# Kernel optimization log

Measured on AMD Instinct MI355X. Metric: run time of the kernel, lower is better.

The kernel has to match this reference:

```python
import jax, jax.numpy as jnp
import numpy as np
import math

L, D, H, DK, DFF, B, S = 4, 512, 8, 256, 2048, 8, 256
HD = H * DK
EPS = 1e-6


def _norm(x, alpha, bias):
    # torch: alpha*(x-mean)/(std_unbiased + eps) + bias  (std uses ddof=1)
    mu = x.mean(axis=-1, keepdims=True)
    var = ((x - mu) ** 2).sum(axis=-1, keepdims=True) / (x.shape[-1] - 1)
    return alpha * (x - mu) / (jnp.sqrt(var) + EPS) + bias


def _positional_encoding():
    pos = jnp.arange(S, dtype=jnp.float32)[:, None]          # [S,1]
    i = jnp.arange(0, D, 2, dtype=jnp.float32)               # even indices
    pe_sin = jnp.sin(pos / (S ** (2.0 * i / D)))             # [S,D/2]
    pe_cos = jnp.cos(pos / (S ** (2.0 * (i + 1.0) / D)))     # [S,D/2]
    pe = jnp.zeros((S, D), dtype=jnp.float32)
    pe = pe.at[:, 0::2].set(pe_sin).at[:, 1::2].set(pe_cos)
    return pe


def setup_inputs() -> dict:
    key = jax.random.key(0)
    ks = jax.random.split(key, 16)
    sc = 0.02
    inp = {
        "data": jax.random.normal(ks[0], (B, S, D), dtype=jnp.float32),
        "attn_m": jax.random.randint(ks[1], (B, S), 0, 2, dtype=jnp.int32),
        "view_idx": 0,
        "seg_emb": jax.random.normal(ks[2], (3, D), dtype=jnp.float32) * sc,
        "Wq": jax.random.normal(ks[3], (L, D, HD), dtype=jnp.float32) * sc,
        "bq": jnp.zeros((L, HD), dtype=jnp.float32),
        "Wk": jax.random.normal(ks[4], (L, D, HD), dtype=jnp.float32) * sc,
        "bk": jnp.zeros((L, HD), dtype=jnp.float32),
        "Wv": jax.random.normal(ks[5], (L, D, HD), dtype=jnp.float32) * sc,
        "bv": jnp.zeros((L, HD), dtype=jnp.float32),
        "Wo": jax.random.normal(ks[6], (L, HD, D), dtype=jnp.float32) * sc,
        "bo": jnp.zeros((L, D), dtype=jnp.float32),
        "W1": jax.random.normal(ks[7], (L, D, DFF), dtype=jnp.float32) * sc,
        "b1": jnp.zeros((L, DFF), dtype=jnp.float32),
        "W2": jax.random.normal(ks[8], (L, DFF, D), dtype=jnp.float32) * sc,
        "b2": jnp.zeros((L, D), dtype=jnp.float32),
        "alpha1": jnp.ones((L, D), dtype=jnp.float32),
        "bias1": jnp.zeros((L, D), dtype=jnp.float32),
        "alpha2": jnp.ones((L, D), dtype=jnp.float32),
        "bias2": jnp.zeros((L, D), dtype=jnp.float32),
        "alpha_f": jnp.ones((D,), dtype=jnp.float32),
        "bias_f": jnp.zeros((D,), dtype=jnp.float32),
    }
    return inp


def reference(data, attn_m, view_idx, seg_emb, Wq, bq, Wk, bk, Wv, bv, Wo, bo,
              W1, b1, W2, b2, alpha1, bias1, alpha2, bias2, alpha_f, bias_f):
    # positional encoder: x*sqrt(d_f) + pe + seg_embedding(view_idx*seq_len)
    pe = _positional_encoding()
    seg_idx = view_idx * S  # scalar; must be < 3 (view_idx == 0 in practice)
    x = data * math.sqrt(D) + pe[None, :, :] + seg_emb[seg_idx][None, None, :]

    # mask: attn_m [B,S] -> [B,1,1,S] bool, True = masked (key axis)
    maskb = attn_m.astype(bool)[:, None, None, :]

    for i in range(L):
        x2 = _norm(x, alpha1[i], bias1[i])
        q = (x2 @ Wq[i] + bq[i]).reshape(B, S, H, DK).transpose(0, 2, 1, 3)
        k = (x2 @ Wk[i] + bk[i]).reshape(B, S, H, DK).transpose(0, 2, 1, 3)
        v = (x2 @ Wv[i] + bv[i]).reshape(B, S, H, DK).transpose(0, 2, 1, 3)
        scores = jnp.einsum('bhqd,bhkd->bhqk', q, k) / math.sqrt(DK)
        scores = jnp.where(maskb, -1e9, scores)
        attnw = jax.nn.softmax(scores, axis=-1)
        o = jnp.einsum('bhqk,bhkd->bhqd', attnw, v)
        o = o.transpose(0, 2, 1, 3).reshape(B, S, HD) @ Wo[i] + bo[i]
        x = x + o
        x2 = _norm(x, alpha2[i], bias2[i])
        ff = jax.nn.relu(x2 @ W1[i] + b1[i]) @ W2[i] + b2[i]
        x = x + ff

    return _norm(x, alpha_f, bias_f)
```

## Files before the change

kernel.cpp:

```cpp
#include <hip/hip_runtime.h>
#include <hip/hip_bf16.h>

#define LNUM 4
#define DIM  512
#define SS   256

typedef unsigned short ushort_t;
typedef __attribute__((ext_vector_type(8))) short bf16x8;
typedef __attribute__((ext_vector_type(4))) float f32x4;
typedef __attribute__((ext_vector_type(8))) unsigned short u16x8;

#define VWAIT(n) asm volatile("s_waitcnt vmcnt(" #n ")" ::: "memory")
#define LWAIT()  asm volatile("s_waitcnt lgkmcnt(0)" ::: "memory")
__device__ __forceinline__ void bar() { __builtin_amdgcn_s_barrier(); }

__device__ __forceinline__ ushort_t f2b(float f) {
  union { float f; unsigned u; } x; x.f = f;
  unsigned r = x.u + 0x7FFFu + ((x.u >> 16) & 1u);
  return (ushort_t)(r >> 16);
}

__device__ __forceinline__ void gload16(const void* g, void* s) {
  __builtin_amdgcn_global_load_lds((const __attribute__((address_space(1))) void*)g,
                                   (__attribute__((address_space(3))) void*)s, 16, 0, 0);
}

template<int TM, int TN, int EPI, int NBUF>
__global__ __launch_bounds__(256, 2)
void gemm_bt(const ushort_t* __restrict__ A, const ushort_t* __restrict__ B,
             const float* __restrict__ bias, const float* __restrict__ bias2,
             const float* __restrict__ bias3,
             ushort_t* __restrict__ outB, ushort_t* __restrict__ outB2,
             ushort_t* __restrict__ outB3, float* __restrict__ outF,
             int K, int lda, int ldb, int ldc, int nkz, int relu)
{
  constexpr int CA = TM / 32, CB = TN / 32, SN = CA + CB;
  constexpr int WM = TM / 32, WN = TN / 32;
  __shared__ ushort_t As[NBUF * TM * 64];
  __shared__ ushort_t Bs[NBUF * TN * 64];
  const int tid = threadIdx.x, lane = tid & 63, wid = tid >> 6;
  const int wm = wid >> 1, wn = wid & 1;
  const int kz = blockIdx.z;
  const int Kz = K / nkz, k0 = kz * Kz, nt = Kz >> 6;

  const ushort_t* Ab = A + (long)blockIdx.y * TM * lda + k0;
  const ushort_t* Bb = B + (long)blockIdx.x * TN * ldb + k0;

  const ushort_t* srcA[CA]; ushort_t* ldsA[CA];
  const ushort_t* srcB[CB]; ushort_t* ldsB[CB];
#pragma unroll
  for (int c = 0; c < CA; ++c) {
    int off = c * 4096 + tid * 16;
    int row = off >> 7;
    int scol = ((off & 127) ^ ((row & 7) << 4)) >> 1;
    srcA[c] = Ab + (long)row * lda + scol;
    ldsA[c] = As + c * 2048 + wid * 512;
  }
#pragma unroll
  for (int c = 0; c < CB; ++c) {
    int off = c * 4096 + tid * 16;
    int row = off >> 7;
    int scol = ((off & 127) ^ ((row & 7) << 4)) >> 1;
    srcB[c] = Bb + (long)row * ldb + scol;
    ldsB[c] = Bs + c * 2048 + wid * 512;
  }

  f32x4 acc[WM][WN] = {};

  auto STAGE = [&](int buf, int t) {
#pragma unroll
    for (int c = 0; c < CA; ++c) gload16(srcA[c] + t * 64, ldsA[c] + buf * TM * 64);
#pragma unroll
    for (int c = 0; c < CB; ++c) gload16(srcB[c] + t * 64, ldsB[c] + buf * TN * 64);
  };

  auto COMPUTE = [&](int buf) {
#pragma unroll
    for (int ks = 0; ks < 2; ++ks) {
      const int kb = ks * 64 + ((lane >> 4) << 4);
      bf16x8 af[WM], bfr[WN];
#pragma unroll
      for (int f = 0; f < WM; ++f) {
        int ra = wm * (TM / 2) + f * 16 + (lane & 15);
        af[f] = *(const bf16x8*)((const char*)As + buf * TM * 128 + ra * 128 + (kb ^ ((ra & 7) << 4)));
      }
#pragma unroll
      for (int g = 0; g < WN; ++g) {
        int rb = wn * (TN / 2) + g * 16 + (lane & 15);
        bfr[g] = *(const bf16x8*)((const char*)Bs + buf * TN * 128 + rb * 128 + (kb ^ ((rb & 7) << 4)));
      }
      __builtin_amdgcn_s_setprio(1);
#pragma unroll
      for (int i = 0; i < WM; ++i)
#pragma unroll
        for (int j = 0; j < WN; ++j)
          acc[i][j] = __builtin_amdgcn_mfma_f32_16x16x32_bf16(af[i], bfr[j], acc[i][j], 0, 0, 0);
      __builtin_amdgcn_s_setprio(0);
    }
  };

  STAGE(0, 0);
  if constexpr (NBUF == 3) {
    STAGE(1, 1);
    for (int t = 0; t < nt; ++t) {
      if (t < nt - 1) { if constexpr (SN == 6) VWAIT(6); else VWAIT(4); }
      else VWAIT(0);
      bar();
      if (t + 2 < nt) STAGE((t + 2) % 3, t + 2);
      COMPUTE(t % 3);
    }
  } else {
    for (int t = 0; t < nt; ++t) {
      VWAIT(0);
      bar();
      if (t + 1 < nt) STAGE((t + 1) & 1, t + 1);
      COMPUTE(t & 1);
    }
  }

  const int row0 = blockIdx.y * TM + wm * (TM / 2) + ((lane >> 4) << 2);
  int col0 = blockIdx.x * TN + wn * (TN / 2) + (lane & 15);
  const float* bsel = bias;
  ushort_t* osel = outB;
  int seg = 0;
  if (EPI == 3) {
    seg = (blockIdx.x * TN) >> 11;
    if (seg == 1) { bsel = bias2; osel = outB2; }
    else if (seg == 2) { bsel = bias3; }
    col0 -= seg * 2048;
  }

  if (EPI == 3 && seg == 2) {
    ushort_t* Vt = As;
    const int colvBase = blockIdx.x * TN - 4096;
    const int rowBase = blockIdx.y * TM;
    const int h = colvBase >> 8, dk0 = colvBase & 255;
    const int bh = ((rowBase >> 8) << 3) + h;
    const int s0 = rowBase & 255;
    bar();
#pragma unroll
    for (int half = 0; half < 2; ++half) {
      if (half) bar();
      if (wn == half) {
#pragma unroll
        for (int i = 0; i < WM; ++i)
#pragma unroll
          for (int j = 0; j < WN; ++j) {
            const int colL = j * 16 + (lane & 15);
            const float bv = bsel[col0 + j * 16];
#pragma unroll
            for (int r = 0; r < 4; ++r) {
              const int rowL = wm * 64 + i * 16 + ((lane >> 4) << 2) + r;
              Vt[colL * 136 + rowL] = f2b(acc[i][j][r] + bv);
            }
          }
      }
      bar();
      const int dkl = tid >> 2, scc = (tid & 3) * 32;
      ushort_t* dst = outB3 + ((long)bh << 16) +
                      (long)(dk0 + half * 64 + dkl) * 256 + s0 + scc;
#pragma unroll
      for (int m = 0; m < 4; ++m)
        *(u16x8*)(dst + m * 8) = *(const u16x8*)(Vt + dkl * 136 + scc + m * 8);
    }
    return;
  }

#pragma unroll
  for (int i = 0; i < WM; ++i) {
#pragma unroll
    for (int j = 0; j < WN; ++j) {
      const int col = col0 + j * 16;
      float bv = 0.f;
      if (EPI == 2) bv = (kz == 0) ? bias[col] : 0.f;
      else if (EPI == 0 || EPI == 3) bv = bsel[col];
#pragma unroll
      for (int r = 0; r < 4; ++r) {
        const int row = row0 + i * 16 + r;
        float v = acc[i][j][r] + bv;
        if (EPI == 2) {
          outF[(long)kz * 1048576 + (long)row * ldc + col] = v;
        } else if (EPI == 3) {
          const long addr = (((long)(row >> 8) * 8 + (col >> 8)) << 16) +
                            (long)(row & 255) * 256 + (col & 255);
          osel[addr] = f2b(v);
        } else {
          if (relu) v = fmaxf(v, 0.f);
          osel[(long)row * ldc + col] = f2b(v);
        }
      }
    }
  }
}

__global__ __launch_bounds__(256, 2)
void attnf_k(const ushort_t* __restrict__ qh, const ushort_t* __restrict__ kh,
             const ushort_t* __restrict__ vT, const int* __restrict__ attnm,
             ushort_t* __restrict__ ao)
{
  __shared__ ushort_t As[2][64 * 64];
  __shared__ ushort_t Bs[2][256 * 64];
  const int bh = blockIdx.x, qt = blockIdx.y;
  const int b = bh >> 3, h = bh & 7;
  const int tid = threadIdx.x, lane = tid & 63, wid = tid >> 6;
  const int l15 = lane & 15, l4 = lane >> 4;

  unsigned mbits = 0;
#pragma unroll
  for (int j = 0; j < 16; ++j)
    mbits |= (attnm[b * 256 + j * 16 + l15] != 0 ? 1u : 0u) << j;

  const ushort_t* Qb = qh + ((long)bh << 16) + qt * 64 * 256;
  const ushort_t* Kb = kh + ((long)bh << 16);
  const ushort_t* srcA[2]; ushort_t* ldsA[2];
  const ushort_t* srcB[8]; ushort_t* ldsB[8];
#pragma unroll
  for (int c = 0; c < 2; ++c) {
    int off = c * 4096 + tid * 16;
    int row = off >> 7;
    int scol = ((off & 127) ^ ((row & 7) << 4)) >> 1;
    srcA[c] = Qb + (long)row * 256 + scol;
    ldsA[c] = As[0] + c * 2048 + wid * 512;
  }
#pragma unroll
  for (int c = 0; c < 8; ++c) {
    int off = c * 4096 + tid * 16;
    int row = off >> 7;
    int scol = ((off & 127) ^ ((row & 7) << 4)) >> 1;
    srcB[c] = Kb + (long)row * 256 + scol;
    ldsB[c] = Bs[0] + c * 2048 + wid * 512;
  }

  auto STAGE = [&](int buf, int t) {
#pragma unroll
    for (int c = 0; c < 2; ++c) gload16(srcA[c] + t * 64, ldsA[c] + buf * 4096);
#pragma unroll
    for (int c = 0; c < 8; ++c) gload16(srcB[c] + t * 64, ldsB[c] + buf * 16384);
  };

  const ushort_t* Vb = vT + ((long)bh << 16);
  int velem[8];
#pragma unroll
  for (int c = 0; c < 8; ++c) {
    int off = c * 4096 + tid * 16;
    int row = off >> 9;
    int colb = (off & 511) ^ ((row & 7) << 4);
    velem[c] = row * 256 + (colb >> 1);
  }
  auto VSTAGE = [&](int buf, int ch) {
#pragma unroll
    for (int c = 0; c < 8; ++c)
      gload16(Vb + (long)ch * 16384 + velem[c], Bs[buf] + c * 2048 + wid * 512);
  };

  f32x4 sacc[16] = {};
  STAGE(0, 0);
  for (int t = 0; t < 4; ++t) {
    VWAIT(0);
    bar();
    if (t < 3) STAGE((t + 1) & 1, t + 1);
    else       VSTAGE(0, 0);
    const int buf = t & 1;
#pragma unroll
    for (int ks = 0; ks < 2; ++ks) {
      const int kb = ks * 64 + (l4 << 4);
      const int ra = wid * 16 + l15;
      bf16x8 af = *(const bf16x8*)((const char*)As[buf] + ra * 128 + (kb ^ ((ra & 7) << 4)));
      __builtin_amdgcn_s_setprio(1);
#pragma unroll
      for (int j = 0; j < 16; ++j) {
        const int rb = j * 16 + l15;
        bf16x8 bf_ = *(const bf16x8*)((const char*)Bs[buf] + rb * 128 + (kb ^ ((rb & 7) << 4)));
        sacc[j] = __builtin_amdgcn_mfma_f32_16x16x32_bf16(af, bf_, sacc[j], 0, 0, 0);
      }
      __builtin_amdgcn_s_setprio(0);
    }
  }

  float mr[4] = {-3e38f, -3e38f, -3e38f, -3e38f}, sr[4] = {};
#pragma unroll
  for (int j = 0; j < 16; ++j) {
    const bool mk = (mbits >> j) & 1;
#pragma unroll
    for (int r = 0; r < 4; ++r) {
      float s = mk ? -1e9f : sacc[j][r] * 0.0625f;
      sacc[j][r] = s;
      mr[r] = fmaxf(mr[r], s);
    }
  }
#pragma unroll
  for (int o = 1; o < 16; o <<= 1)
#pragma unroll
    for (int r = 0; r < 4; ++r) mr[r] = fmaxf(mr[r], __shfl_xor(mr[r], o, 16));
#pragma unroll
  for (int j = 0; j < 16; ++j)
#pragma unroll
    for (int r = 0; r < 4; ++r) {
      float e = __expf(sacc[j][r] - mr[r]);
      sacc[j][r] = e;
      sr[r] += e;
    }
#pragma unroll
  for (int o = 1; o < 16; o <<= 1)
#pragma unroll
    for (int r = 0; r < 4; ++r) sr[r] += __shfl_xor(sr[r], o, 16);
#pragma unroll
  for (int r = 0; r < 4; ++r) sr[r] = 1.f / sr[r];

  bar();
  ushort_t* Rp = (ushort_t*)Bs[1];
#pragma unroll
  for (int j = 0; j < 16; ++j)
#pragma unroll
    for (int r = 0; r < 4; ++r) {
      const int row = wid * 16 + l4 * 4 + r;
      *(ushort_t*)((char*)Rp + row * 512 + (((j * 16 + l15) * 2) ^ ((row & 7) << 4))) =
          f2b(sacc[j][r] * sr[r]);
    }
  bf16x8 pf[8];
  {
    const int ra = wid * 16 + l15;
#pragma unroll
    for (int ks = 0; ks < 8; ++ks)
      pf[ks] = *(const bf16x8*)((const char*)Rp + ra * 512 +
                                ((ks * 64 + (l4 << 4)) ^ ((ra & 7) << 4)));
  }
  LWAIT();
  VWAIT(0);
  bar();

  f32x4 oacc[16] = {};
  for (int ch = 0; ch < 4; ++ch) {
    if (ch) { VWAIT(0); bar(); }
    if (ch < 3) VSTAGE((ch + 1) & 1, ch + 1);
    const char* vb = (const char*)Bs[ch & 1];
#pragma unroll
    for (int ks = 0; ks < 8; ++ks) {
      const int kb = ks * 64 + (l4 << 4);
      __builtin_amdgcn_s_setprio(1);
#pragma unroll
      for (int j = 0; j < 4; ++j) {
        const int rb = j * 16 + l15;
        bf16x8 vf = *(const bf16x8*)(vb + rb * 512 + (kb ^ ((rb & 7) << 4)));
        oacc[ch * 4 + j] = __builtin_amdgcn_mfma_f32_16x16x32_bf16(pf[ks], vf, oacc[ch * 4 + j], 0, 0, 0);
      }
      __builtin_amdgcn_s_setprio(0);
    }
  }

  const int rowq = qt * 64 + wid * 16 + (l4 << 2);
#pragma unroll
  for (int ch = 0; ch < 4; ++ch)
#pragma unroll
    for (int j = 0; j < 4; ++j) {
      const int dk = ch * 64 + j * 16 + l15;
#pragma unroll
      for (int r = 0; r < 4; ++r)
        ao[(long)(b * 256 + rowq + r) * 2048 + h * 256 + dk] = f2b(oacc[ch * 4 + j][r]);
    }
}

__global__ __launch_bounds__(256)
void build_ln(const float* __restrict__ data, const float* __restrict__ seg,
              const int* __restrict__ viewp,
              const float* __restrict__ alpha, const float* __restrict__ beta,
              float* __restrict__ x, ushort_t* __restrict__ x2)
{
  const int row = blockIdx.x, tid = threadIdx.x;
  const long base = (long)row * DIM;
  const int s = row & 255;
  const int vrow = viewp[0] * SS;
  const int d0 = tid * 2;
  float2 v;
  {
    float2 dv = ((const float2*)(data + base))[tid];
    float a0 = (float)s * exp2f((float)d0 * -0.03125f);
    float a1 = (float)s * exp2f((float)(d0 + 1) * -0.03125f);
    float pe0 = (d0 & 1) ? cosf(a0) : sinf(a0);
    float pe1 = ((d0 + 1) & 1) ? cosf(a1) : sinf(a1);
    v.x = dv.x * 22.627416997969522f + pe0 + seg[vrow * DIM + d0];
    v.y = dv.y * 22.627416997969522f + pe1 + seg[vrow * DIM + d0 + 1];
    ((float2*)(x + base))[tid] = v;
  }
  float sm = v.x + v.y;
#pragma unroll
  for (int o = 32; o; o >>= 1) sm += __shfl_xor(sm, o, 64);
  __shared__ float rs[4], rq[4];
  if ((tid & 63) == 0) rs[tid >> 6] = sm;
  __syncthreads();
  const float mu = (rs[0] + rs[1] + rs[2] + rs[3]) * (1.f / 512.f);
  const float dx = v.x - mu, dy = v.y - mu;
  float q = dx * dx + dy * dy;
#pragma unroll
  for (int o = 32; o; o >>= 1) q += __shfl_xor(q, o, 64);
  if ((tid & 63) == 0) rq[tid >> 6] = q;
  __syncthreads();
  const float var = (rq[0] + rq[1] + rq[2] + rq[3]) * (1.f / 511.f);
  const float rstd = 1.f / (sqrtf(var) + 1e-6f);
  x2[base + d0]     = f2b(alpha[d0] * dx * rstd + beta[d0]);
  x2[base + d0 + 1] = f2b(alpha[d0 + 1] * dy * rstd + beta[d0 + 1]);
}

__global__ __launch_bounds__(256)
void lnorm_k(const float* __restrict__ x, const float* __restrict__ parts, int np,
             float* __restrict__ xout,
             const float* __restrict__ alpha, const float* __restrict__ beta,
             ushort_t* __restrict__ outB, float* __restrict__ outF)
{
  const int row = blockIdx.x, tid = threadIdx.x;
  const long base = (long)row * DIM;
  float2 v = ((const float2*)(x + base))[tid];
  if (np) {
    for (int p = 0; p < np; ++p) {
      float2 a = ((const float2*)(parts + (long)p * 1048576 + base))[tid];
      v.x += a.x; v.y += a.y;
    }
    ((float2*)(xout + base))[tid] = v;
  }
  float s = v.x + v.y;
#pragma unroll
  for (int o = 32; o; o >>= 1) s += __shfl_xor(s, o, 64);
  __shared__ float rs[4], rq[4];
  if ((tid & 63) == 0) rs[tid >> 6] = s;
  __syncthreads();
  const float mu = (rs[0] + rs[1] + rs[2] + rs[3]) * (1.f / 512.f);
  const float dx = v.x - mu, dy = v.y - mu;
  float q = dx * dx + dy * dy;
#pragma unroll
  for (int o = 32; o; o >>= 1) q += __shfl_xor(q, o, 64);
  if ((tid & 63) == 0) rq[tid >> 6] = q;
  __syncthreads();
  const float var = (rq[0] + rq[1] + rq[2] + rq[3]) * (1.f / 511.f);
  const float rstd = 1.f / (sqrtf(var) + 1e-6f);
  const int d0 = tid * 2;
  const float o0 = alpha[d0] * dx * rstd + beta[d0];
  const float o1 = alpha[d0 + 1] * dy * rstd + beta[d0 + 1];
  if (outB) { outB[base + d0] = f2b(o0); outB[base + d0 + 1] = f2b(o1); }
  else      { outF[base + d0] = o0;      outF[base + d0 + 1] = o1; }
}

__global__ __launch_bounds__(256)
void wtransA(const float* __restrict__ Wq, const float* __restrict__ Wk,
             const float* __restrict__ Wv, const float* __restrict__ W1,
             ushort_t* __restrict__ qkvW, ushort_t* __restrict__ W1T)
{
  __shared__ float t[32][33];
  const int z = blockIdx.z, widx = z >> 2, layer = z & 3;
  const float* src = (widx == 0) ? Wq : (widx == 1) ? Wk : (widx == 2) ? Wv : W1;
  src += (long)layer * 512 * 2048;
  ushort_t* dst = (widx == 3) ? (W1T + (long)layer * 2048 * 512)
                              : (qkvW + (long)layer * (6144L * 512) + (long)widx * 2048 * 512);
  const int c0 = blockIdx.x * 32, r0 = blockIdx.y * 32;
  const int tx = threadIdx.x & 31, ty = threadIdx.x >> 5;
#pragma unroll
  for (int i = 0; i < 4; ++i) t[ty + i * 8][tx] = src[(long)(r0 + ty + i * 8) * 2048 + c0 + tx];
  __syncthreads();
#pragma unroll
  for (int i = 0; i < 4; ++i) dst[(long)(c0 + ty + i * 8) * 512 + r0 + tx] = f2b(t[tx][ty + i * 8]);
}

__global__ __launch_bounds__(256)
void wtransB(const float* __restrict__ Wo, const float* __restrict__ W2,
             ushort_t* __restrict__ WoT, ushort_t* __restrict__ W2T)
{
  __shared__ float t[32][33];
  const int z = blockIdx.z, widx = z >> 2, layer = z & 3;
  const float* src = ((widx == 0) ? Wo : W2) + (long)layer * 2048 * 512;
  ushort_t* dst = ((widx == 0) ? WoT : W2T) + (long)layer * 512 * 2048;
  const int c0 = blockIdx.x * 32, r0 = blockIdx.y * 32;
  const int tx = threadIdx.x & 31, ty = threadIdx.x >> 5;
#pragma unroll
  for (int i = 0; i < 4; ++i) t[ty + i * 8][tx] = src[(long)(r0 + ty + i * 8) * 512 + c0 + tx];
  __syncthreads();
#pragma unroll
  for (int i = 0; i < 4; ++i) dst[(long)(c0 + ty + i * 8) * 2048 + r0 + tx] = f2b(t[tx][ty + i * 8]);
}

extern "C" void kernel_launch(void* const* d_in, const int* in_sizes, int n_in,
                              void* d_out, int out_size, void* d_ws, size_t ws_size,
                              hipStream_t stream)
{
  const float* data  = (const float*)d_in[0];
  const int*   attnm = (const int*)d_in[1];
  const int*   viewp = (const int*)d_in[2];
  const float* seg   = (const float*)d_in[3];
  const float* Wq    = (const float*)d_in[4];
  const float* bq    = (const float*)d_in[5];
  const float* Wk    = (const float*)d_in[6];
  const float* bk    = (const float*)d_in[7];
  const float* Wv    = (const float*)d_in[8];
  const float* bv    = (const float*)d_in[9];
  const float* Wo    = (const float*)d_in[10];
  const float* bo    = (const float*)d_in[11];
  const float* W1    = (const float*)d_in[12];
  const float* b1    = (const float*)d_in[13];
  const float* W2    = (const float*)d_in[14];
  const float* b2    = (const float*)d_in[15];
  const float* al1   = (const float*)d_in[16];
  const float* be1   = (const float*)d_in[17];
  const float* al2   = (const float*)d_in[18];
  const float* be2   = (const float*)d_in[19];
  const float* alf   = (const float*)d_in[20];
  const float* bef   = (const float*)d_in[21];

  char* w = (char*)d_ws;
  const size_t MB = 1024 * 1024;
  ushort_t* qkvW = (ushort_t*)(w + 0 * MB);
  ushort_t* WoT  = (ushort_t*)(w + 24 * MB);
  ushort_t* W1T  = (ushort_t*)(w + 32 * MB);
  ushort_t* W2T  = (ushort_t*)(w + 40 * MB);
  float*    x    = (float*)   (w + 48 * MB);
  ushort_t* x2   = (ushort_t*)(w + 52 * MB);
  ushort_t* qb   = (ushort_t*)(w + 54 * MB);
  ushort_t* kbf  = (ushort_t*)(w + 62 * MB);
  ushort_t* vT   = (ushort_t*)(w + 70 * MB);
  ushort_t* ao   = (ushort_t*)(w + 78 * MB);
  ushort_t* ffh  = (ushort_t*)(w + 86 * MB);
  float*    parts= (float*)   (w + 94 * MB);

  dim3 blk(256);
  const long QKV_L = 6144L * 512;
  wtransA<<<dim3(64, 16, 16), blk, 0, stream>>>(Wq, Wk, Wv, W1, qkvW, W1T);
  wtransB<<<dim3(16, 64, 8), blk, 0, stream>>>(Wo, W2, WoT, W2T);
  build_ln<<<2048, blk, 0, stream>>>(data, seg, viewp, al1, be1, x, x2);

  for (int i = 0; i < LNUM; ++i) {
    gemm_bt<128, 128, 3, 2><<<dim3(48, 16, 1), blk, 0, stream>>>(
        x2, qkvW + (long)i * QKV_L, bq + i * 2048, bk + i * 2048, bv + i * 2048,
        qb, kbf, vT, nullptr, 512, 512, 512, 2048, 1, 0);
    attnf_k<<<dim3(64, 4), blk, 0, stream>>>(qb, kbf, vT, attnm, ao);
    gemm_bt<64, 64, 2, 3><<<dim3(8, 32, 2), blk, 0, stream>>>(
        ao, WoT + (long)i * 512 * 2048, bo + i * 512, nullptr, nullptr,
        nullptr, nullptr, nullptr, parts, 2048, 2048, 2048, 512, 2, 0);
    lnorm_k<<<2048, blk, 0, stream>>>(x, parts, 2, x, al2 + i * 512, be2 + i * 512, x2, nullptr);
    gemm_bt<128, 64, 0, 3><<<dim3(32, 16, 1), blk, 0, stream>>>(
        x2, W1T + (long)i * 2048 * 512, b1 + i * 2048, nullptr, nullptr,
        ffh, nullptr, nullptr, nullptr, 512, 512, 512, 2048, 1, 1);
    gemm_bt<64, 64, 2, 3><<<dim3(8, 32, 2), blk, 0, stream>>>(
        ffh, W2T + (long)i * 512 * 2048, b2 + i * 512, nullptr, nullptr,
        nullptr, nullptr, nullptr, parts, 2048, 2048, 2048, 512, 2, 0);
    if (i < LNUM - 1)
      lnorm_k<<<2048, blk, 0, stream>>>(x, parts, 2, x, al1 + (i + 1) * 512, be1 + (i + 1) * 512, x2, nullptr);
    else
      lnorm_k<<<2048, blk, 0, stream>>>(x, parts, 2, x, alf, bef, nullptr, (float*)d_out);
  }
}
```

Baseline: 396.8 us.

## Drop split-K for output GEMMs and fuse residual add into epilogue

Removes the two-way split-K on the Wo and W2 projections. The GEMM epilogue now adds its result (plus bias) directly into the fp32 residual stream x with a read-modify-write. Layernorm no longer sums partial buffers or writes x back. This removes the partial-sum write/read traffic and one buffer, at the cost of halving the grid (256 blocks) and doubling each block's K loop.

```diff
diff --git a/kernel.cpp b/kernel.cpp
--- a/kernel.cpp
+++ b/kernel.cpp
@@ -32,7 +32,7 @@
              const float* __restrict__ bias3,
              ushort_t* __restrict__ outB, ushort_t* __restrict__ outB2,
              ushort_t* __restrict__ outB3, float* __restrict__ outF,
-             int K, int lda, int ldb, int ldc, int nkz, int relu)
+             int K, int lda, int ldb, int ldc, int relu)
 {
   constexpr int CA = TM / 32, CB = TN / 32, SN = CA + CB;
   constexpr int WM = TM / 32, WN = TN / 32;
@@ -40,11 +40,10 @@
   __shared__ ushort_t Bs[NBUF * TN * 64];
   const int tid = threadIdx.x, lane = tid & 63, wid = tid >> 6;
   const int wm = wid >> 1, wn = wid & 1;
-  const int kz = blockIdx.z;
-  const int Kz = K / nkz, k0 = kz * Kz, nt = Kz >> 6;
-
-  const ushort_t* Ab = A + (long)blockIdx.y * TM * lda + k0;
-  const ushort_t* Bb = B + (long)blockIdx.x * TN * ldb + k0;
+  const int nt = K >> 6;
+
+  const ushort_t* Ab = A + (long)blockIdx.y * TM * lda;
+  const ushort_t* Bb = B + (long)blockIdx.x * TN * ldb;
 
   const ushort_t* srcA[CA]; ushort_t* ldsA[CA];
   const ushort_t* srcB[CB]; ushort_t* ldsB[CB];
@@ -172,14 +171,14 @@
     for (int j = 0; j < WN; ++j) {
       const int col = col0 + j * 16;
       float bv = 0.f;
-      if (EPI == 2) bv = (kz == 0) ? bias[col] : 0.f;
-      else if (EPI == 0 || EPI == 3) bv = bsel[col];
+      if (EPI == 2 || EPI == 0 || EPI == 3) bv = bsel[col];
 #pragma unroll
       for (int r = 0; r < 4; ++r) {
         const int row = row0 + i * 16 + r;
         float v = acc[i][j][r] + bv;
         if (EPI == 2) {
-          outF[(long)kz * 1048576 + (long)row * ldc + col] = v;
+          float* p = outF + (long)row * ldc + col;
+          *p = *p + v;
         } else if (EPI == 3) {
           const long addr = (((long)(row >> 8) * 8 + (col >> 8)) << 16) +
                             (long)(row & 255) * 256 + (col & 255);
@@ -402,21 +401,13 @@
 }
 
 __global__ __launch_bounds__(256)
-void lnorm_k(const float* __restrict__ x, const float* __restrict__ parts, int np,
-             float* __restrict__ xout,
+void lnorm_k(const float* __restrict__ x,
              const float* __restrict__ alpha, const float* __restrict__ beta,
              ushort_t* __restrict__ outB, float* __restrict__ outF)
 {
   const int row = blockIdx.x, tid = threadIdx.x;
   const long base = (long)row * DIM;
   float2 v = ((const float2*)(x + base))[tid];
-  if (np) {
-    for (int p = 0; p < np; ++p) {
-      float2 a = ((const float2*)(parts + (long)p * 1048576 + base))[tid];
-      v.x += a.x; v.y += a.y;
-    }
-    ((float2*)(xout + base))[tid] = v;
-  }
   float s = v.x + v.y;
 #pragma unroll
   for (int o = 32; o; o >>= 1) s += __shfl_xor(s, o, 64);
@@ -516,7 +507,6 @@
   ushort_t* vT   = (ushort_t*)(w + 70 * MB);
   ushort_t* ao   = (ushort_t*)(w + 78 * MB);
   ushort_t* ffh  = (ushort_t*)(w + 86 * MB);
-  float*    parts= (float*)   (w + 94 * MB);
 
   dim3 blk(256);
   const long QKV_L = 6144L * 512;
@@ -527,21 +517,21 @@
   for (int i = 0; i < LNUM; ++i) {
     gemm_bt<128, 128, 3, 2><<<dim3(48, 16, 1), blk, 0, stream>>>(
         x2, qkvW + (long)i * QKV_L, bq + i * 2048, bk + i * 2048, bv + i * 2048,
-        qb, kbf, vT, nullptr, 512, 512, 512, 2048, 1, 0);
+        qb, kbf, vT, nullptr, 512, 512, 512, 2048, 0);
     attnf_k<<<dim3(64, 4), blk, 0, stream>>>(qb, kbf, vT, attnm, ao);
-    gemm_bt<64, 64, 2, 3><<<dim3(8, 32, 2), blk, 0, stream>>>(
+    gemm_bt<64, 64, 2, 3><<<dim3(8, 32, 1), blk, 0, stream>>>(
         ao, WoT + (long)i * 512 * 2048, bo + i * 512, nullptr, nullptr,
-        nullptr, nullptr, nullptr, parts, 2048, 2048, 2048, 512, 2, 0);
-    lnorm_k<<<2048, blk, 0, stream>>>(x, parts, 2, x, al2 + i * 512, be2 + i * 512, x2, nullptr);
+        nullptr, nullptr, nullptr, x, 2048, 2048, 2048, 512, 0);
+    lnorm_k<<<2048, blk, 0, stream>>>(x, al2 + i * 512, be2 + i * 512, x2, nullptr);
     gemm_bt<128, 64, 0, 3><<<dim3(32, 16, 1), blk, 0, stream>>>(
         x2, W1T + (long)i * 2048 * 512, b1 + i * 2048, nullptr, nullptr,
-        ffh, nullptr, nullptr, nullptr, 512, 512, 512, 2048, 1, 1);
-    gemm_bt<64, 64, 2, 3><<<dim3(8, 32, 2), blk, 0, stream>>>(
+        ffh, nullptr, nullptr, nullptr, 512, 512, 512, 2048, 1);
+    gemm_bt<64, 64, 2, 3><<<dim3(8, 32, 1), blk, 0, stream>>>(
         ffh, W2T + (long)i * 512 * 2048, b2 + i * 512, nullptr, nullptr,
-        nullptr, nullptr, nullptr, parts, 2048, 2048, 2048, 512, 2, 0);
+        nullptr, nullptr, nullptr, x, 2048, 2048, 2048, 512, 0);
     if (i < LNUM - 1)
-      lnorm_k<<<2048, blk, 0, stream>>>(x, parts, 2, x, al1 + (i + 1) * 512, be1 + (i + 1) * 512, x2, nullptr);
+      lnorm_k<<<2048, blk, 0, stream>>>(x, al1 + (i + 1) * 512, be1 + (i + 1) * 512, x2, nullptr);
     else
-      lnorm_k<<<2048, blk, 0, stream>>>(x, parts, 2, x, alf, bef, nullptr, (float*)d_out);
-  }
-}
+      lnorm_k<<<2048, blk, 0, stream>>>(x, alf, bef, nullptr, (float*)d_out);
+  }
+}
```

Measured after the change: 467.9 us. 1.18x slower.
